# Kernel optimization log

Hardware: AMD Instinct MI355X
Metric: run time of the kernel (lower is better)

Reference implementation:

```python
import jax, jax.numpy as jnp
import numpy as np

GENETIC_CODE = {'TTT': 'F', 'TTC': 'F', 'TTA': 'L', 'TTG': 'L', 'CTT': 'L', 'CTC': 'L', 'CTA': 'L', 'CTG': 'L', 'ATT': 'I', 'ATC': 'I', 'ATA': 'I', 'ATG': 'M', 'GTT': 'V', 'GTC': 'V', 'GTA': 'V', 'GTG': 'V', 'TCT': 'S', 'TCC': 'S', 'TCA': 'S', 'TCG': 'S', 'AGT': 'S', 'AGC': 'S', 'CCT': 'P', 'CCC': 'P', 'CCA': 'P', 'CCG': 'P', 'ACT': 'T', 'ACC': 'T', 'ACA': 'T', 'ACG': 'T', 'GCT': 'A', 'GCC': 'A', 'GCA': 'A', 'GCG': 'A', 'TAT': 'Y', 'TAC': 'Y', 'TAA': '*', 'TAG': '*', 'TGA': '*', 'CAT': 'H', 'CAC': 'H', 'CAA': 'Q', 'CAG': 'Q', 'AAT': 'N', 'AAC': 'N', 'AAA': 'K', 'AAG': 'K', 'GAT': 'D', 'GAC': 'D', 'GAA': 'E', 'GAG': 'E', 'TGT': 'C', 'TGC': 'C', 'TGG': 'W', 'CGT': 'R', 'CGC': 'R', 'CGA': 'R', 'CGG': 'R', 'AGA': 'R', 'AGG': 'R', 'GGT': 'G', 'GGC': 'G', 'GGA': 'G', 'GGG': 'G'}
NUC_TO_IDX = {'T': 0, 'C': 1, 'A': 2, 'G': 3}

def _build_syn_bias(synonymy_bias=1.0):
    idx = lambda c: NUC_TO_IDX[c[0]] * 16 + NUC_TO_IDX[c[1]] * 4 + NUC_TO_IDX[c[2]]
    groups = {}
    for codon, aa in GENETIC_CODE.items():
        groups.setdefault(aa, []).append(idx(codon))
    m = np.zeros((64, 64), dtype=np.float32)
    for codons in groups.values():
        for i in codons:
            for j in codons:
                m[i, j] = synonymy_bias
    return jnp.asarray(m)

HIDDEN, N_HEADS = 256, 4
HEAD_DIM = HIDDEN // N_HEADS
B, S = 2, 4096

def setup_inputs() -> dict:
    key = jax.random.key(0)
    ks = jax.random.split(key, 10)
    std = 1.0 / np.sqrt(HIDDEN)
    lin = lambda k: jax.random.uniform(k, (HIDDEN, HIDDEN), jnp.float32, -std, std)
    bias = lambda k: jax.random.uniform(k, (HIDDEN,), jnp.float32, -std, std)
    return {
        'x': jax.random.normal(ks[0], (B, S, HIDDEN), jnp.float32),
        'codons': jax.random.randint(ks[1], (B, S), 0, 64),
        'syn_bias': _build_syn_bias(1.0),
        'wq': lin(ks[2]), 'bq': bias(ks[3]),
        'wk': lin(ks[4]), 'bk': bias(ks[5]),
        'wv': lin(ks[6]), 'bv': bias(ks[7]),
        'wo': lin(ks[8]), 'bo': bias(ks[9]),
    }

def reference(x, codons, syn_bias, wq, bq, wk, bk, wv, bv, wo, bo):
    b, s, _ = x.shape
    split = lambda t: t.reshape(b, s, N_HEADS, HEAD_DIM).transpose(0, 2, 1, 3)  # (B,H,S,D)
    q = split(x @ wq.T + bq)
    k = split(x @ wk.T + bk)
    v = split(x @ wv.T + bv)
    scores = jnp.einsum('bhqd,bhkd->bhqk', q, k) / np.sqrt(HEAD_DIM)
    # gather pairwise synonymy bias: (B,S,S) broadcast over heads
    pair_bias = syn_bias[codons[:, :, None], codons[:, None, :]]
    scores = scores + pair_bias[:, None, :, :]
    attn = jax.nn.softmax(scores, axis=-1)
    out = jnp.einsum('bhqk,bhkd->bhqd', attn, v)
    out = out.transpose(0, 2, 1, 3).reshape(b, s, HIDDEN)
    return out @ wo.T + bo
```

## Files before the change

kernel.cpp:

```cpp
#include <hip/hip_runtime.h>
#include <hip/hip_bf16.h>

#define NH 4
#define HD 64
#define HID 256
#define SS 4096
#define KP 96

#define QFRAG_PER_HEAD (128 * 6 * 64 * 8)
#define KFRAG_PER_HEAD (64 * 12 * 64 * 8)
#define VFRAG_PER_HEAD (64 * 8 * 64 * 8)

typedef float f4 __attribute__((ext_vector_type(4)));
typedef float f16v __attribute__((ext_vector_type(16)));
typedef short bf8 __attribute__((ext_vector_type(8)));
typedef unsigned int u4v __attribute__((ext_vector_type(4)));

static __device__ __forceinline__ float fast_exp2(float x) {
#if __has_builtin(__builtin_amdgcn_exp2f)
    return __builtin_amdgcn_exp2f(x);
#else
    float r; asm("v_exp_f32 %0, %1" : "=v"(r) : "v"(x)); return r;
#endif
}

static __device__ __forceinline__ unsigned pack2(float a, float b) {
    unsigned ua = (unsigned)__bfloat16_as_ushort(__float2bfloat16(a));
    unsigned ub = (unsigned)__bfloat16_as_ushort(__float2bfloat16(b));
    return ua | (ub << 16);
}

__global__ void setup_kernel(const float* __restrict__ syn,
                             int* __restrict__ gid, float* __restrict__ betaP)
{
    const int lane = threadIdx.x;
    int rep = 64;
    for (int j = 63; j >= 0; --j)
        if (syn[lane * 64 + j] != 0.0f) rep = j;
    if (rep == 64) rep = lane;
    unsigned long long m = __ballot(rep == lane);
    int id = (int)__popcll(m & ((2ull << rep) - 1ull)) - 1;
    if (id < 0) id = 0;
    gid[lane] = id;
    if (lane == 0) *betaP = syn[0] * 1.44269504088896f;
}

__global__ __launch_bounds__(256)
void pack_w_kernel(const float* __restrict__ wq, const float* __restrict__ wk,
                   const float* __restrict__ wv, const float* __restrict__ wo,
                   __hip_bfloat16* __restrict__ wpk)
{
    const int t = blockIdx.x * 256 + threadIdx.x;
    const int mat = t >> 13;
    const int r = t & 8191;
    const int dt = r >> 10, ks = (r >> 6) & 15, lane = r & 63;
    const float* w = (mat == 0) ? wq : (mat == 1) ? wk : (mat == 2) ? wv : wo;
    const int row = dt * 32 + (lane & 31);
    const int col = ks * 16 + (lane >> 5) * 8;
    const f4 a = *(const f4*)&w[(size_t)row * 256 + col];
    const f4 b = *(const f4*)&w[(size_t)row * 256 + col + 4];
    union { unsigned u[4]; bf8 v; } o;
    o.u[0] = pack2(a[0], a[1]); o.u[1] = pack2(a[2], a[3]);
    o.u[2] = pack2(b[0], b[1]); o.u[3] = pack2(b[2], b[3]);
    *(bf8*)&wpk[(size_t)t * 8] = o.v;
}

__global__ __launch_bounds__(256)
void qkv_mfma_kernel(const float* __restrict__ x,
                     const __hip_bfloat16* __restrict__ wpk,
                     const float* __restrict__ bq, const float* __restrict__ bk,
                     const float* __restrict__ bv,
                     const int* __restrict__ codons,
                     const int* __restrict__ gid, const float* __restrict__ betaP,
                     __hip_bfloat16* __restrict__ qfrag,
                     __hip_bfloat16* __restrict__ kfrag,
                     __hip_bfloat16* __restrict__ vfrag)
{
    const int bid = blockIdx.x;
    const int stile = bid / 6;
    const int grp = bid % 6;
    const int tid = threadIdx.x;
    const int w = tid >> 6, lane = tid & 63, hi = lane >> 5, l5 = lane & 31;

    const int bidx = stile >> 7;
    const int stl = stile & 127;
    const int hs = stl & 1, tkv = stl >> 1;

    __shared__ __hip_bfloat16 xs[32][256];

    {
        const int r0 = tid >> 5, c = tid & 31;
        #pragma unroll
        for (int it = 0; it < 4; ++it) {
            const int row = r0 + it * 8;
            const f4 a = *(const f4*)&x[(size_t)(stile * 32 + row) * HID + c * 8];
            const f4 b2 = *(const f4*)&x[(size_t)(stile * 32 + row) * HID + c * 8 + 4];
            union { unsigned u[4]; bf8 v; } o;
            o.u[0] = pack2(a[0], a[1]); o.u[1] = pack2(a[2], a[3]);
            o.u[2] = pack2(b2[0], b2[1]); o.u[3] = pack2(b2[2], b2[3]);
            *(bf8*)&xs[row][((c ^ row) & 31) * 8] = o.v;
        }
    }
    __syncthreads();

    const int t24 = grp * 4 + w;
    const int mat = t24 >> 3;
    const int dt = t24 & 7;
    const int head = dt >> 1, d32 = dt & 1;

    const __hip_bfloat16* wb = wpk + (size_t)((mat * 8 + dt) * 16) * 512 + (size_t)lane * 8;
    bf8 wf[16];
    #pragma unroll
    for (int ks = 0; ks < 16; ++ks) wf[ks] = *(const bf8*)&wb[ks * 512];

    f16v acc;
    #pragma unroll
    for (int r = 0; r < 16; ++r) acc[r] = 0.0f;

    if (mat < 2) {
        #pragma unroll
        for (int ks = 0; ks < 16; ++ks) {
            const bf8 xf = *(const bf8*)&xs[l5][(((ks * 2 + hi) ^ l5) & 31) * 8];
            acc = __builtin_amdgcn_mfma_f32_32x32x16_bf16(wf[ks], xf, acc, 0, 0, 0);
        }
    } else {
        #pragma unroll
        for (int ks = 0; ks < 16; ++ks) {
            const bf8 xf = *(const bf8*)&xs[l5][(((ks * 2 + hi) ^ l5) & 31) * 8];
            acc = __builtin_amdgcn_mfma_f32_32x32x16_bf16(xf, wf[ks], acc, 0, 0, 0);
        }
    }

    const float QSCALE = 0.18033688011112042f;
    if (mat == 0) {
        f4 b4[4];
        #pragma unroll
        for (int j = 0; j < 4; ++j)
            b4[j] = *(const f4*)&bq[head * 64 + d32 * 32 + j * 8 + 4 * hi];
        #pragma unroll
        for (int r = 0; r < 16; ++r) acc[r] = (acc[r] + b4[r >> 2][r & 3]) * QSCALE;
    } else if (mat == 1) {
        f4 b4[4];
        #pragma unroll
        for (int j = 0; j < 4; ++j)
            b4[j] = *(const f4*)&bk[head * 64 + d32 * 32 + j * 8 + 4 * hi];
        #pragma unroll
        for (int r = 0; r < 16; ++r) acc[r] += b4[r >> 2][r & 3];
    } else {
        const float bn = bv[head * 64 + d32 * 32 + l5];
        #pragma unroll
        for (int r = 0; r < 16; ++r) acc[r] += bn;
    }

    unsigned wd[8];
    #pragma unroll
    for (int i = 0; i < 8; ++i) wd[i] = pack2(acc[2 * i], acc[2 * i + 1]);
    const unsigned e0 = (unsigned)__shfl_xor((int)(hi ? wd[0] : wd[2]), 32, 64);
    const unsigned e1 = (unsigned)__shfl_xor((int)(hi ? wd[1] : wd[3]), 32, 64);
    const unsigned e2 = (unsigned)__shfl_xor((int)(hi ? wd[4] : wd[6]), 32, 64);
    const unsigned e3 = (unsigned)__shfl_xor((int)(hi ? wd[5] : wd[7]), 32, 64);
    union { unsigned u[4]; bf8 v; } fa, fb;
    if (hi == 0) {
        fa.u[0] = wd[0]; fa.u[1] = wd[1]; fa.u[2] = e0; fa.u[3] = e1;
        fb.u[0] = wd[4]; fb.u[1] = wd[5]; fb.u[2] = e2; fb.u[3] = e3;
    } else {
        fa.u[0] = e0; fa.u[1] = e1; fa.u[2] = wd[2]; fa.u[3] = wd[3];
        fb.u[0] = e2; fb.u[1] = e3; fb.u[2] = wd[6]; fb.u[3] = wd[7];
    }

    const int hd = bidx * NH + head;
    if (mat == 0) {
        __hip_bfloat16* qb = qfrag + (size_t)hd * QFRAG_PER_HEAD;
        *(bf8*)&qb[((size_t)(stl * 6 + d32 * 2 + 0) * 64 + lane) * 8] = fa.v;
        *(bf8*)&qb[((size_t)(stl * 6 + d32 * 2 + 1) * 64 + lane) * 8] = fb.v;
    } else if (mat == 1) {
        __hip_bfloat16* kb = kfrag + (size_t)hd * KFRAG_PER_HEAD;
        *(bf8*)&kb[((size_t)(tkv * 12 + d32 * 4 + hs) * 64 + lane) * 8] = fa.v;
        *(bf8*)&kb[((size_t)(tkv * 12 + d32 * 4 + 2 + hs) * 64 + lane) * 8] = fb.v;
    } else {
        __hip_bfloat16* vb = vfrag + (size_t)hd * VFRAG_PER_HEAD;
        const int ja = ((stl * 2 + 0) & 3) * 2 + d32;
        const int jb = ((stl * 2 + 1) & 3) * 2 + d32;
        *(bf8*)&vb[((size_t)(tkv * 8 + ja) * 64 + lane) * 8] = fa.v;
        *(bf8*)&vb[((size_t)(tkv * 8 + jb) * 64 + lane) * 8] = fb.v;
    }

    if (grp == 0) {
        const int hh = w;
        const int hd2 = bidx * NH + hh;
        __hip_bfloat16* qb = qfrag + (size_t)hd2 * QFRAG_PER_HEAD;
        __hip_bfloat16* kb = kfrag + (size_t)hd2 * KFRAG_PER_HEAD;
        u4v z; z[0] = 0; z[1] = 0; z[2] = 0; z[3] = 0;
        *(u4v*)&qb[((size_t)(stl * 6 + 4) * 64 + lane) * 8] = z;
        *(u4v*)&qb[((size_t)(stl * 6 + 5) * 64 + lane) * 8] = z;
        *(u4v*)&kb[((size_t)(tkv * 12 + 8 + hs) * 64 + lane) * 8] = z;
        *(u4v*)&kb[((size_t)(tkv * 12 + 10 + hs) * 64 + lane) * 8] = z;
        asm volatile("s_waitcnt vmcnt(0)" ::: "memory");
        if (hi == 0) {
            const int cg = gid[codons[bidx * SS + stl * 32 + l5] & 63];
            const float bl2e = *betaP;
            const int lt = ((cg >> 3) & 1) * 32 + l5;
            qb[((size_t)(stl * 6 + 4 + (cg >> 4)) * 64 + lt) * 8 + (cg & 7)] =
                __float2bfloat16(bl2e);
            kb[((size_t)(tkv * 12 + 8 + (cg >> 4) * 2 + hs) * 64 + lt) * 8 + (cg & 7)] =
                __float2bfloat16(1.0f);
        }
    }
}

__global__ __launch_bounds__(256, 2)
void attn_kernel(const __hip_bfloat16* __restrict__ qfrag,
                 const __hip_bfloat16* __restrict__ kfrag,
                 const __hip_bfloat16* __restrict__ vfrag,
                 __hip_bfloat16* __restrict__ aoutb)
{
    const int bid = blockIdx.x;
    const int bh = bid & 7;
    const int b = bh >> 2, h = bh & 3;
    const int qtile = bid >> 3;
    const int tid = threadIdx.x;
    const int w = tid >> 6;
    const int lane = tid & 63;
    const int q5 = lane & 31;
    const int hi = lane >> 5;

    __shared__ float o_sh[4][32][69];
    __shared__ float l_sh[4][32];

    const __hip_bfloat16* kf_base = kfrag + (size_t)(b * NH + h) * KFRAG_PER_HEAD + lane * 8;
    const __hip_bfloat16* vf_base = vfrag + (size_t)(b * NH + h) * VFRAG_PER_HEAD + lane * 8;

    const __hip_bfloat16* qb = qfrag + (size_t)(b * NH + h) * QFRAG_PER_HEAD
                               + ((size_t)qtile * 6 * 64 + lane) * 8;
    bf8 qf[6];
    #pragma unroll
    for (int ks = 0; ks < 6; ++ks)
        qf[ks] = *(const bf8*)&qb[ks * 512];

    f16v oacc0, oacc1;
    #pragma unroll
    for (int r = 0; r < 16; ++r) { oacc0[r] = 0.0f; oacc1[r] = 0.0f; }
    float lrun = 0.0f;

    bf8 kA[12], kB[12];

    auto loadK = [&](bf8 (&dst)[12], int tt) {
        const __hip_bfloat16* p = kf_base + (size_t)tt * (12 * 64 * 8);
        #pragma unroll
        for (int j = 0; j < 12; ++j) dst[j] = *(const bf8*)&p[j * 512];
    };

    auto step = [&](bf8 (&kf)[12], bf8 (&kn)[12], int tt, bool pf) {
        bf8 vf[8];
        const __hip_bfloat16* vp = vf_base + (size_t)tt * (8 * 64 * 8);
        #pragma unroll
        for (int j = 0; j < 8; ++j) vf[j] = *(const bf8*)&vp[j * 512];
        if (pf) loadK(kn, tt + 1);

        f16v sA, sB;
        #pragma unroll
        for (int r = 0; r < 16; ++r) { sA[r] = 0.0f; sB[r] = 0.0f; }
        __builtin_amdgcn_s_setprio(1);
        #pragma unroll
        for (int ks = 0; ks < 6; ++ks) {
            sA = __builtin_amdgcn_mfma_f32_32x32x16_bf16(kf[ks * 2 + 0], qf[ks], sA, 0, 0, 0);
            sB = __builtin_amdgcn_mfma_f32_32x32x16_bf16(kf[ks * 2 + 1], qf[ks], sB, 0, 0, 0);
        }
        __builtin_amdgcn_s_setprio(0);

        float ls = 0.0f;
        #pragma unroll
        for (int r = 0; r < 16; ++r) { sA[r] = fast_exp2(sA[r]); ls += sA[r]; }
        #pragma unroll
        for (int r = 0; r < 16; ++r) { sB[r] = fast_exp2(sB[r]); ls += sB[r]; }
        lrun += ls;

        unsigned dwv[2][4][2];
        #pragma unroll
        for (int j = 0; j < 4; ++j)
            #pragma unroll
            for (int c = 0; c < 2; ++c) {
                dwv[0][j][c] = pack2(sA[j * 4 + 2 * c], sA[j * 4 + 2 * c + 1]);
                dwv[1][j][c] = pack2(sB[j * 4 + 2 * c], sB[j * 4 + 2 * c + 1]);
            }
        unsigned rc[2][2][2];
        #pragma unroll
        for (int t2 = 0; t2 < 2; ++t2)
            #pragma unroll
            for (int k1 = 0; k1 < 2; ++k1)
                #pragma unroll
                for (int c = 0; c < 2; ++c) {
                    const unsigned snd = hi ? dwv[t2][2 * k1][c] : dwv[t2][2 * k1 + 1][c];
                    rc[t2][k1][c] = (unsigned)__shfl_xor((int)snd, 32, 64);
                }

        __builtin_amdgcn_s_setprio(1);
        #pragma unroll
        for (int ks = 0; ks < 4; ++ks) {
            const int t2 = ks >> 1, k1 = ks & 1;
            union { unsigned u[4]; bf8 v; } pfv;
            pfv.u[0] = hi ? rc[t2][k1][0] : dwv[t2][2 * k1][0];
            pfv.u[1] = hi ? rc[t2][k1][1] : dwv[t2][2 * k1][1];
            pfv.u[2] = hi ? dwv[t2][2 * k1 + 1][0] : rc[t2][k1][0];
            pfv.u[3] = hi ? dwv[t2][2 * k1 + 1][1] : rc[t2][k1][1];
            oacc0 = __builtin_amdgcn_mfma_f32_32x32x16_bf16(vf[ks * 2 + 0], pfv.v, oacc0, 0, 0, 0);
            oacc1 = __builtin_amdgcn_mfma_f32_32x32x16_bf16(vf[ks * 2 + 1], pfv.v, oacc1, 0, 0, 0);
        }
        __builtin_amdgcn_s_setprio(0);
    };

    const int tt0 = w * 16;
    loadK(kA, tt0);
    #pragma unroll 1
    for (int t = 0; t < 16; t += 2) {
        step(kA, kB, tt0 + t, true);
        step(kB, kA, tt0 + t + 1, t + 2 < 16);
    }

    const float ltot = lrun + __shfl_xor(lrun, 32, 64);
    #pragma unroll
    for (int r = 0; r < 16; ++r) {
        const int d = (r & 3) + 8 * (r >> 2) + 4 * hi;
        o_sh[w][q5][d] = oacc0[r];
        o_sh[w][q5][32 + d] = oacc1[r];
    }
    if (hi == 0) l_sh[w][q5] = ltot;
    __syncthreads();

    const int row = tid >> 3;
    const int d0 = (tid & 7) * 8;
    const float inv = 1.0f / (l_sh[0][row] + l_sh[1][row] + l_sh[2][row] + l_sh[3][row]);
    float vals[8];
    #pragma unroll
    for (int j = 0; j < 8; ++j)
        vals[j] = (o_sh[0][row][d0 + j] + o_sh[1][row][d0 + j]
                 + o_sh[2][row][d0 + j] + o_sh[3][row][d0 + j]) * inv;
    union { unsigned u[4]; bf8 v; } ov;
    ov.u[0] = pack2(vals[0], vals[1]); ov.u[1] = pack2(vals[2], vals[3]);
    ov.u[2] = pack2(vals[4], vals[5]); ov.u[3] = pack2(vals[6], vals[7]);
    *(bf8*)&aoutb[((size_t)b * SS + qtile * 32 + row) * HID + h * HD + d0] = ov.v;
}

__global__ __launch_bounds__(256)
void out_proj_kernel(const __hip_bfloat16* __restrict__ aoutb,
                     const __hip_bfloat16* __restrict__ wpk,
                     const float* __restrict__ bo, float* __restrict__ out)
{
    const int bid = blockIdx.x;
    const int stile = bid >> 1, grp = bid & 1;
    const int tid = threadIdx.x;
    const int w = tid >> 6, lane = tid & 63, hi = lane >> 5, l5 = lane & 31;

    __shared__ __hip_bfloat16 xs[32][256];
    {
        const int r0 = tid >> 5, c = tid & 31;
        #pragma unroll
        for (int it = 0; it < 4; ++it) {
            const int row = r0 + it * 8;
            const bf8 v = *(const bf8*)&aoutb[(size_t)(stile * 32 + row) * HID + c * 8];
            *(bf8*)&xs[row][((c ^ row) & 31) * 8] = v;
        }
    }
    __syncthreads();

    const int nt = grp * 4 + w;
    const __hip_bfloat16* wb = wpk + (size_t)((3 * 8 + nt) * 16) * 512 + (size_t)lane * 8;
    bf8 wf[16];
    #pragma unroll
    for (int ks = 0; ks < 16; ++ks) wf[ks] = *(const bf8*)&wb[ks * 512];

    f16v acc;
    #pragma unroll
    for (int r = 0; r < 16; ++r) acc[r] = 0.0f;
    #pragma unroll
    for (int ks = 0; ks < 16; ++ks) {
        const bf8 xf = *(const bf8*)&xs[l5][(((ks * 2 + hi) ^ l5) & 31) * 8];
        acc = __builtin_amdgcn_mfma_f32_32x32x16_bf16(xf, wf[ks], acc, 0, 0, 0);
    }

    const float bn = bo[nt * 32 + l5];
    #pragma unroll
    for (int r = 0; r < 16; ++r) {
        const int sloc = (r & 3) + 8 * (r >> 2) + 4 * hi;
        out[(size_t)(stile * 32 + sloc) * HID + nt * 32 + l5] = acc[r] + bn;
    }
}

extern "C" void kernel_launch(void* const* d_in, const int* in_sizes, int n_in,
                              void* d_out, int out_size, void* d_ws, size_t ws_size,
                              hipStream_t stream)
{
    (void)in_sizes; (void)n_in; (void)out_size; (void)ws_size;
    const float* x        = (const float*)d_in[0];
    const int*   codons   = (const int*)d_in[1];
    const float* syn_bias = (const float*)d_in[2];
    const float* wq = (const float*)d_in[3];
    const float* bq = (const float*)d_in[4];
    const float* wk = (const float*)d_in[5];
    const float* bk = (const float*)d_in[6];
    const float* wv = (const float*)d_in[7];
    const float* bv = (const float*)d_in[8];
    const float* wo = (const float*)d_in[9];
    const float* bo = (const float*)d_in[10];
    float* out = (float*)d_out;

    char* ws = (char*)d_ws;
    int*   gid   = (int*)(ws);
    float* betaP = (float*)(ws + 256);
    __hip_bfloat16* wpk   = (__hip_bfloat16*)(ws + 4096);
    __hip_bfloat16* qfrag = (__hip_bfloat16*)(ws + (size_t)1048576u);
    __hip_bfloat16* kfrag = (__hip_bfloat16*)(ws + (size_t)7340032u);
    __hip_bfloat16* vfrag = (__hip_bfloat16*)(ws + (size_t)13631488u);
    __hip_bfloat16* aoutb = (__hip_bfloat16*)(ws + (size_t)17825792u);

    setup_kernel<<<1, 64, 0, stream>>>(syn_bias, gid, betaP);
    pack_w_kernel<<<128, 256, 0, stream>>>(wq, wk, wv, wo, wpk);
    qkv_mfma_kernel<<<1536, 256, 0, stream>>>(x, wpk, bq, bk, bv, codons, gid, betaP,
                                              qfrag, kfrag, vfrag);
    attn_kernel<<<1024, 256, 0, stream>>>(qfrag, kfrag, vfrag, aoutb);
    out_proj_kernel<<<512, 256, 0, stream>>>(aoutb, wpk, bo, out);
}
```

Measured before the change: 90.93 us.

## Process two query tiles per attention block to reuse K/V fragments

Each attention block now handles 64 queries (two 32-row tiles) instead of 32. Every loaded K and V fragment feeds both tiles, which halves global K/V traffic per query, and the grid shrinks from 1024 to 512 blocks. The K double buffer is replaced by a single buffer that is refilled after the second score MFMA. The trade-off is more accumulator registers, a larger shared-memory reduction buffer, and fewer blocks, which may lower occupancy and latency hiding.

```diff
diff --git a/kernel.cpp b/kernel.cpp
--- a/kernel.cpp
+++ b/kernel.cpp
@@ -217,64 +217,45 @@
     const int bid = blockIdx.x;
     const int bh = bid & 7;
     const int b = bh >> 2, h = bh & 3;
-    const int qtile = bid >> 3;
+    const int qg = bid >> 3;
     const int tid = threadIdx.x;
     const int w = tid >> 6;
     const int lane = tid & 63;
     const int q5 = lane & 31;
     const int hi = lane >> 5;
 
-    __shared__ float o_sh[4][32][69];
-    __shared__ float l_sh[4][32];
+    __shared__ float o_sh[4][64][69];
+    __shared__ float l_sh[4][64];
 
     const __hip_bfloat16* kf_base = kfrag + (size_t)(b * NH + h) * KFRAG_PER_HEAD + lane * 8;
     const __hip_bfloat16* vf_base = vfrag + (size_t)(b * NH + h) * VFRAG_PER_HEAD + lane * 8;
 
     const __hip_bfloat16* qb = qfrag + (size_t)(b * NH + h) * QFRAG_PER_HEAD
-                               + ((size_t)qtile * 6 * 64 + lane) * 8;
-    bf8 qf[6];
-    #pragma unroll
-    for (int ks = 0; ks < 6; ++ks)
-        qf[ks] = *(const bf8*)&qb[ks * 512];
-
-    f16v oacc0, oacc1;
-    #pragma unroll
-    for (int r = 0; r < 16; ++r) { oacc0[r] = 0.0f; oacc1[r] = 0.0f; }
-    float lrun = 0.0f;
-
-    bf8 kA[12], kB[12];
-
-    auto loadK = [&](bf8 (&dst)[12], int tt) {
+                               + ((size_t)(qg * 2) * 6 * 64 + lane) * 8;
+    bf8 qf0[6], qf1[6];
+    #pragma unroll
+    for (int ks = 0; ks < 6; ++ks) {
+        qf0[ks] = *(const bf8*)&qb[ks * 512];
+        qf1[ks] = *(const bf8*)&qb[3072 + ks * 512];
+    }
+
+    f16v oacc00, oacc01, oacc10, oacc11;
+    #pragma unroll
+    for (int r = 0; r < 16; ++r) {
+        oacc00[r] = 0.0f; oacc01[r] = 0.0f; oacc10[r] = 0.0f; oacc11[r] = 0.0f;
+    }
+    float lrun0 = 0.0f, lrun1 = 0.0f;
+
+    bf8 kf[12];
+    const int tt0 = w * 16;
+
+    auto loadK = [&](int tt) {
         const __hip_bfloat16* p = kf_base + (size_t)tt * (12 * 64 * 8);
         #pragma unroll
-        for (int j = 0; j < 12; ++j) dst[j] = *(const bf8*)&p[j * 512];
+        for (int j = 0; j < 12; ++j) kf[j] = *(const bf8*)&p[j * 512];
     };
 
-    auto step = [&](bf8 (&kf)[12], bf8 (&kn)[12], int tt, bool pf) {
-        bf8 vf[8];
-        const __hip_bfloat16* vp = vf_base + (size_t)tt * (8 * 64 * 8);
-        #pragma unroll
-        for (int j = 0; j < 8; ++j) vf[j] = *(const bf8*)&vp[j * 512];
-        if (pf) loadK(kn, tt + 1);
-
-        f16v sA, sB;
-        #pragma unroll
-        for (int r = 0; r < 16; ++r) { sA[r] = 0.0f; sB[r] = 0.0f; }
-        __builtin_amdgcn_s_setprio(1);
-        #pragma unroll
-        for (int ks = 0; ks < 6; ++ks) {
-            sA = __builtin_amdgcn_mfma_f32_32x32x16_bf16(kf[ks * 2 + 0], qf[ks], sA, 0, 0, 0);
-            sB = __builtin_amdgcn_mfma_f32_32x32x16_bf16(kf[ks * 2 + 1], qf[ks], sB, 0, 0, 0);
-        }
-        __builtin_amdgcn_s_setprio(0);
-
-        float ls = 0.0f;
-        #pragma unroll
-        for (int r = 0; r < 16; ++r) { sA[r] = fast_exp2(sA[r]); ls += sA[r]; }
-        #pragma unroll
-        for (int r = 0; r < 16; ++r) { sB[r] = fast_exp2(sB[r]); ls += sB[r]; }
-        lrun += ls;
-
+    auto packP = [&](const f16v& sA, const f16v& sB, bf8 (&pfv)[4]) {
         unsigned dwv[2][4][2];
         #pragma unroll
         for (int j = 0; j < 4; ++j)
@@ -293,52 +274,110 @@
                     const unsigned snd = hi ? dwv[t2][2 * k1][c] : dwv[t2][2 * k1 + 1][c];
                     rc[t2][k1][c] = (unsigned)__shfl_xor((int)snd, 32, 64);
                 }
-
-        __builtin_amdgcn_s_setprio(1);
         #pragma unroll
         for (int ks = 0; ks < 4; ++ks) {
             const int t2 = ks >> 1, k1 = ks & 1;
-            union { unsigned u[4]; bf8 v; } pfv;
-            pfv.u[0] = hi ? rc[t2][k1][0] : dwv[t2][2 * k1][0];
-            pfv.u[1] = hi ? rc[t2][k1][1] : dwv[t2][2 * k1][1];
-            pfv.u[2] = hi ? dwv[t2][2 * k1 + 1][0] : rc[t2][k1][0];
-            pfv.u[3] = hi ? dwv[t2][2 * k1 + 1][1] : rc[t2][k1][1];
-            oacc0 = __builtin_amdgcn_mfma_f32_32x32x16_bf16(vf[ks * 2 + 0], pfv.v, oacc0, 0, 0, 0);
-            oacc1 = __builtin_amdgcn_mfma_f32_32x32x16_bf16(vf[ks * 2 + 1], pfv.v, oacc1, 0, 0, 0);
+            union { unsigned u[4]; bf8 v; } pu;
+            pu.u[0] = hi ? rc[t2][k1][0] : dwv[t2][2 * k1][0];
+            pu.u[1] = hi ? rc[t2][k1][1] : dwv[t2][2 * k1][1];
+            pu.u[2] = hi ? dwv[t2][2 * k1 + 1][0] : rc[t2][k1][0];
+            pu.u[3] = hi ? dwv[t2][2 * k1 + 1][1] : rc[t2][k1][1];
+            pfv[ks] = pu.v;
+        }
+    };
+
+    loadK(tt0);
+
+    #pragma unroll 1
+    for (int t = 0; t < 16; ++t) {
+        const int tt = tt0 + t;
+
+        bf8 vf[8];
+        const __hip_bfloat16* vp = vf_base + (size_t)tt * (8 * 64 * 8);
+        #pragma unroll
+        for (int j = 0; j < 8; ++j) vf[j] = *(const bf8*)&vp[j * 512];
+
+        f16v sA, sB;
+        #pragma unroll
+        for (int r = 0; r < 16; ++r) { sA[r] = 0.0f; sB[r] = 0.0f; }
+        __builtin_amdgcn_s_setprio(1);
+        #pragma unroll
+        for (int ks = 0; ks < 6; ++ks) {
+            sA = __builtin_amdgcn_mfma_f32_32x32x16_bf16(kf[ks * 2 + 0], qf0[ks], sA, 0, 0, 0);
+            sB = __builtin_amdgcn_mfma_f32_32x32x16_bf16(kf[ks * 2 + 1], qf0[ks], sB, 0, 0, 0);
         }
         __builtin_amdgcn_s_setprio(0);
-    };
-
-    const int tt0 = w * 16;
-    loadK(kA, tt0);
-    #pragma unroll 1
-    for (int t = 0; t < 16; t += 2) {
-        step(kA, kB, tt0 + t, true);
-        step(kB, kA, tt0 + t + 1, t + 2 < 16);
-    }
-
-    const float ltot = lrun + __shfl_xor(lrun, 32, 64);
+
+        float ls0 = 0.0f;
+        #pragma unroll
+        for (int r = 0; r < 16; ++r) { sA[r] = fast_exp2(sA[r]); ls0 += sA[r]; }
+        #pragma unroll
+        for (int r = 0; r < 16; ++r) { sB[r] = fast_exp2(sB[r]); ls0 += sB[r]; }
+        lrun0 += ls0;
+        bf8 pfv0[4];
+        packP(sA, sB, pfv0);
+
+        #pragma unroll
+        for (int r = 0; r < 16; ++r) { sA[r] = 0.0f; sB[r] = 0.0f; }
+        __builtin_amdgcn_s_setprio(1);
+        #pragma unroll
+        for (int ks = 0; ks < 6; ++ks) {
+            sA = __builtin_amdgcn_mfma_f32_32x32x16_bf16(kf[ks * 2 + 0], qf1[ks], sA, 0, 0, 0);
+            sB = __builtin_amdgcn_mfma_f32_32x32x16_bf16(kf[ks * 2 + 1], qf1[ks], sB, 0, 0, 0);
+        }
+        __builtin_amdgcn_s_setprio(0);
+
+        if (t + 1 < 16) loadK(tt + 1);
+
+        float ls1 = 0.0f;
+        #pragma unroll
+        for (int r = 0; r < 16; ++r) { sA[r] = fast_exp2(sA[r]); ls1 += sA[r]; }
+        #pragma unroll
+        for (int r = 0; r < 16; ++r) { sB[r] = fast_exp2(sB[r]); ls1 += sB[r]; }
+        lrun1 += ls1;
+        bf8 pfv1[4];
+        packP(sA, sB, pfv1);
+
+        __builtin_amdgcn_s_setprio(1);
+        #pragma unroll
+        for (int ks = 0; ks < 4; ++ks) {
+            oacc00 = __builtin_amdgcn_mfma_f32_32x32x16_bf16(vf[ks * 2 + 0], pfv0[ks], oacc00, 0, 0, 0);
+            oacc01 = __builtin_amdgcn_mfma_f32_32x32x16_bf16(vf[ks * 2 + 1], pfv0[ks], oacc01, 0, 0, 0);
+            oacc10 = __builtin_amdgcn_mfma_f32_32x32x16_bf16(vf[ks * 2 + 0], pfv1[ks], oacc10, 0, 0, 0);
+            oacc11 = __builtin_amdgcn_mfma_f32_32x32x16_bf16(vf[ks * 2 + 1], pfv1[ks], oacc11, 0, 0, 0);
+        }
+        __builtin_amdgcn_s_setprio(0);
+    }
+
+    const float ltot0 = lrun0 + __shfl_xor(lrun0, 32, 64);
+    const float ltot1 = lrun1 + __shfl_xor(lrun1, 32, 64);
     #pragma unroll
     for (int r = 0; r < 16; ++r) {
         const int d = (r & 3) + 8 * (r >> 2) + 4 * hi;
-        o_sh[w][q5][d] = oacc0[r];
-        o_sh[w][q5][32 + d] = oacc1[r];
-    }
-    if (hi == 0) l_sh[w][q5] = ltot;
+        o_sh[w][q5][d] = oacc00[r];
+        o_sh[w][q5][32 + d] = oacc01[r];
+        o_sh[w][32 + q5][d] = oacc10[r];
+        o_sh[w][32 + q5][32 + d] = oacc11[r];
+    }
+    if (hi == 0) { l_sh[w][q5] = ltot0; l_sh[w][32 + q5] = ltot1; }
     __syncthreads();
 
-    const int row = tid >> 3;
-    const int d0 = (tid & 7) * 8;
+    const int row = tid >> 2;
+    const int d0 = (tid & 3) * 16;
     const float inv = 1.0f / (l_sh[0][row] + l_sh[1][row] + l_sh[2][row] + l_sh[3][row]);
-    float vals[8];
-    #pragma unroll
-    for (int j = 0; j < 8; ++j)
+    float vals[16];
+    #pragma unroll
+    for (int j = 0; j < 16; ++j)
         vals[j] = (o_sh[0][row][d0 + j] + o_sh[1][row][d0 + j]
                  + o_sh[2][row][d0 + j] + o_sh[3][row][d0 + j]) * inv;
-    union { unsigned u[4]; bf8 v; } ov;
-    ov.u[0] = pack2(vals[0], vals[1]); ov.u[1] = pack2(vals[2], vals[3]);
-    ov.u[2] = pack2(vals[4], vals[5]); ov.u[3] = pack2(vals[6], vals[7]);
-    *(bf8*)&aoutb[((size_t)b * SS + qtile * 32 + row) * HID + h * HD + d0] = ov.v;
+    union { unsigned u[4]; bf8 v; } ov0, ov1;
+    ov0.u[0] = pack2(vals[0], vals[1]);   ov0.u[1] = pack2(vals[2], vals[3]);
+    ov0.u[2] = pack2(vals[4], vals[5]);   ov0.u[3] = pack2(vals[6], vals[7]);
+    ov1.u[0] = pack2(vals[8], vals[9]);   ov1.u[1] = pack2(vals[10], vals[11]);
+    ov1.u[2] = pack2(vals[12], vals[13]); ov1.u[3] = pack2(vals[14], vals[15]);
+    __hip_bfloat16* dst = &aoutb[((size_t)b * SS + qg * 64 + row) * HID + h * HD + d0];
+    *(bf8*)&dst[0] = ov0.v;
+    *(bf8*)&dst[8] = ov1.v;
 }
 
 __global__ __launch_bounds__(256)
@@ -417,6 +456,6 @@
     pack_w_kernel<<<128, 256, 0, stream>>>(wq, wk, wv, wo, wpk);
     qkv_mfma_kernel<<<1536, 256, 0, stream>>>(x, wpk, bq, bk, bv, codons, gid, betaP,
                                               qfrag, kfrag, vfrag);
-    attn_kernel<<<1024, 256, 0, stream>>>(qfrag, kfrag, vfrag, aoutb);
+    attn_kernel<<<512, 256, 0, stream>>>(qfrag, kfrag, vfrag, aoutb);
     out_proj_kernel<<<512, 256, 0, stream>>>(aoutb, wpk, bo, out);
 }
```

Measured after the change: 102.8 us. 1.13x slower.

## Share K/V tiles across waves via LDS and split KV range into two halves

Applied to the files above, without the earlier changes.

The attention kernel now has each wave own a separate 32-query tile. The four waves cooperatively stage each K/V tile into double-buffered shared memory, replacing per-wave global reloads of the same K/V fragments. The key range is split across two blocks that write unnormalized bf16 partial outputs and row sums. The output projection sums these partials and normalizes them. This cuts redundant global K/V traffic by sharing it across waves, at the cost of per-tile __syncthreads, extra LDS reads, and a second partial buffer with extra bf16 rounding of the unnormalized sums.

```diff
diff --git a/kernel.cpp b/kernel.cpp
--- a/kernel.cpp
+++ b/kernel.cpp
@@ -5,7 +5,6 @@
 #define HD 64
 #define HID 256
 #define SS 4096
-#define KP 96
 
 #define QFRAG_PER_HEAD (128 * 6 * 64 * 8)
 #define KFRAG_PER_HEAD (64 * 12 * 64 * 8)
@@ -212,50 +211,73 @@
 void attn_kernel(const __hip_bfloat16* __restrict__ qfrag,
                  const __hip_bfloat16* __restrict__ kfrag,
                  const __hip_bfloat16* __restrict__ vfrag,
-                 __hip_bfloat16* __restrict__ aoutb)
+                 __hip_bfloat16* __restrict__ po0,
+                 __hip_bfloat16* __restrict__ po1,
+                 float* __restrict__ ls0,
+                 float* __restrict__ ls1)
 {
     const int bid = blockIdx.x;
     const int bh = bid & 7;
     const int b = bh >> 2, h = bh & 3;
-    const int qtile = bid >> 3;
+    const int idx = bid >> 3;
+    const int half = idx & 1;
+    const int qg = idx >> 1;
     const int tid = threadIdx.x;
     const int w = tid >> 6;
     const int lane = tid & 63;
     const int q5 = lane & 31;
     const int hi = lane >> 5;
 
-    __shared__ float o_sh[4][32][69];
-    __shared__ float l_sh[4][32];
-
-    const __hip_bfloat16* kf_base = kfrag + (size_t)(b * NH + h) * KFRAG_PER_HEAD + lane * 8;
-    const __hip_bfloat16* vf_base = vfrag + (size_t)(b * NH + h) * VFRAG_PER_HEAD + lane * 8;
-
+    __shared__ __align__(16) char smem[40960];
+    __shared__ float l_sh[128];
+
+    const char* kT = (const char*)(kfrag + (size_t)(b * NH + h) * KFRAG_PER_HEAD);
+    const char* vT = (const char*)(vfrag + (size_t)(b * NH + h) * VFRAG_PER_HEAD);
+
+    const int stl = qg * 4 + w;
     const __hip_bfloat16* qb = qfrag + (size_t)(b * NH + h) * QFRAG_PER_HEAD
-                               + ((size_t)qtile * 6 * 64 + lane) * 8;
+                               + ((size_t)stl * 6 * 64 + lane) * 8;
     bf8 qf[6];
     #pragma unroll
-    for (int ks = 0; ks < 6; ++ks)
-        qf[ks] = *(const bf8*)&qb[ks * 512];
+    for (int ks = 0; ks < 6; ++ks) qf[ks] = *(const bf8*)&qb[ks * 512];
 
     f16v oacc0, oacc1;
     #pragma unroll
     for (int r = 0; r < 16; ++r) { oacc0[r] = 0.0f; oacc1[r] = 0.0f; }
     float lrun = 0.0f;
 
-    bf8 kA[12], kB[12];
-
-    auto loadK = [&](bf8 (&dst)[12], int tt) {
-        const __hip_bfloat16* p = kf_base + (size_t)tt * (12 * 64 * 8);
-        #pragma unroll
-        for (int j = 0; j < 12; ++j) dst[j] = *(const bf8*)&p[j * 512];
+    const int w5 = w * 5;
+    bf8 g[5];
+
+    auto loadG = [&](int tt) {
+        #pragma unroll
+        for (int c = 0; c < 5; ++c) {
+            const int id = w5 + c;
+            const char* src = (id < 12)
+                ? kT + (size_t)tt * 12288 + (size_t)id * 1024
+                : vT + (size_t)tt * 8192 + (size_t)(id - 12) * 1024;
+            g[c] = *(const bf8*)(src + lane * 16);
+        }
     };
-
-    auto step = [&](bf8 (&kf)[12], bf8 (&kn)[12], int tt, bool pf) {
-        bf8 vf[8];
-        const __hip_bfloat16* vp = vf_base + (size_t)tt * (8 * 64 * 8);
-        #pragma unroll
-        for (int j = 0; j < 8; ++j) vf[j] = *(const bf8*)&vp[j * 512];
-        if (pf) loadK(kn, tt + 1);
+    auto writeL = [&](int buf) {
+        #pragma unroll
+        for (int c = 0; c < 5; ++c) {
+            const int id = w5 + c;
+            *(bf8*)&smem[buf * 20480 + id * 1024 + lane * 16] = g[c];
+        }
+    };
+
+    const int tt0 = half * 32;
+    loadG(tt0);
+    writeL(0);
+    __syncthreads();
+
+    int cur = 0;
+    #pragma unroll 1
+    for (int t = 0; t < 32; ++t) {
+        if (t + 1 < 32) loadG(tt0 + t + 1);
+
+        const char* kb = smem + cur * 20480 + lane * 16;
 
         f16v sA, sB;
         #pragma unroll
@@ -263,8 +285,10 @@
         __builtin_amdgcn_s_setprio(1);
         #pragma unroll
         for (int ks = 0; ks < 6; ++ks) {
-            sA = __builtin_amdgcn_mfma_f32_32x32x16_bf16(kf[ks * 2 + 0], qf[ks], sA, 0, 0, 0);
-            sB = __builtin_amdgcn_mfma_f32_32x32x16_bf16(kf[ks * 2 + 1], qf[ks], sB, 0, 0, 0);
+            const bf8 k0 = *(const bf8*)(kb + (2 * ks) * 1024);
+            const bf8 k1 = *(const bf8*)(kb + (2 * ks + 1) * 1024);
+            sA = __builtin_amdgcn_mfma_f32_32x32x16_bf16(k0, qf[ks], sA, 0, 0, 0);
+            sB = __builtin_amdgcn_mfma_f32_32x32x16_bf16(k1, qf[ks], sB, 0, 0, 0);
         }
         __builtin_amdgcn_s_setprio(0);
 
@@ -293,56 +317,67 @@
                     const unsigned snd = hi ? dwv[t2][2 * k1][c] : dwv[t2][2 * k1 + 1][c];
                     rc[t2][k1][c] = (unsigned)__shfl_xor((int)snd, 32, 64);
                 }
-
-        __builtin_amdgcn_s_setprio(1);
+        bf8 pfv[4];
         #pragma unroll
         for (int ks = 0; ks < 4; ++ks) {
             const int t2 = ks >> 1, k1 = ks & 1;
-            union { unsigned u[4]; bf8 v; } pfv;
-            pfv.u[0] = hi ? rc[t2][k1][0] : dwv[t2][2 * k1][0];
-            pfv.u[1] = hi ? rc[t2][k1][1] : dwv[t2][2 * k1][1];
-            pfv.u[2] = hi ? dwv[t2][2 * k1 + 1][0] : rc[t2][k1][0];
-            pfv.u[3] = hi ? dwv[t2][2 * k1 + 1][1] : rc[t2][k1][1];
-            oacc0 = __builtin_amdgcn_mfma_f32_32x32x16_bf16(vf[ks * 2 + 0], pfv.v, oacc0, 0, 0, 0);
-            oacc1 = __builtin_amdgcn_mfma_f32_32x32x16_bf16(vf[ks * 2 + 1], pfv.v, oacc1, 0, 0, 0);
+            union { unsigned u[4]; bf8 v; } pu;
+            pu.u[0] = hi ? rc[t2][k1][0] : dwv[t2][2 * k1][0];
+            pu.u[1] = hi ? rc[t2][k1][1] : dwv[t2][2 * k1][1];
+            pu.u[2] = hi ? dwv[t2][2 * k1 + 1][0] : rc[t2][k1][0];
+            pu.u[3] = hi ? dwv[t2][2 * k1 + 1][1] : rc[t2][k1][1];
+            pfv[ks] = pu.v;
+        }
+
+        __builtin_amdgcn_s_setprio(1);
+        #pragma unroll
+        for (int ks = 0; ks < 4; ++ks) {
+            const bf8 v0 = *(const bf8*)(kb + (12 + 2 * ks) * 1024);
+            const bf8 v1 = *(const bf8*)(kb + (13 + 2 * ks) * 1024);
+            oacc0 = __builtin_amdgcn_mfma_f32_32x32x16_bf16(v0, pfv[ks], oacc0, 0, 0, 0);
+            oacc1 = __builtin_amdgcn_mfma_f32_32x32x16_bf16(v1, pfv[ks], oacc1, 0, 0, 0);
         }
         __builtin_amdgcn_s_setprio(0);
-    };
-
-    const int tt0 = w * 16;
-    loadK(kA, tt0);
-    #pragma unroll 1
-    for (int t = 0; t < 16; t += 2) {
-        step(kA, kB, tt0 + t, true);
-        step(kB, kA, tt0 + t + 1, t + 2 < 16);
+
+        if (t + 1 < 32) writeL(cur ^ 1);
+        __syncthreads();
+        cur ^= 1;
     }
 
     const float ltot = lrun + __shfl_xor(lrun, 32, 64);
+    float* osh = (float*)smem;
     #pragma unroll
     for (int r = 0; r < 16; ++r) {
         const int d = (r & 3) + 8 * (r >> 2) + 4 * hi;
-        o_sh[w][q5][d] = oacc0[r];
-        o_sh[w][q5][32 + d] = oacc1[r];
-    }
-    if (hi == 0) l_sh[w][q5] = ltot;
+        osh[(w * 32 + q5) * 68 + d] = oacc0[r];
+        osh[(w * 32 + q5) * 68 + 32 + d] = oacc1[r];
+    }
+    if (hi == 0) l_sh[w * 32 + q5] = ltot;
     __syncthreads();
 
-    const int row = tid >> 3;
-    const int d0 = (tid & 7) * 8;
-    const float inv = 1.0f / (l_sh[0][row] + l_sh[1][row] + l_sh[2][row] + l_sh[3][row]);
-    float vals[8];
-    #pragma unroll
-    for (int j = 0; j < 8; ++j)
-        vals[j] = (o_sh[0][row][d0 + j] + o_sh[1][row][d0 + j]
-                 + o_sh[2][row][d0 + j] + o_sh[3][row][d0 + j]) * inv;
-    union { unsigned u[4]; bf8 v; } ov;
-    ov.u[0] = pack2(vals[0], vals[1]); ov.u[1] = pack2(vals[2], vals[3]);
-    ov.u[2] = pack2(vals[4], vals[5]); ov.u[3] = pack2(vals[6], vals[7]);
-    *(bf8*)&aoutb[((size_t)b * SS + qtile * 32 + row) * HID + h * HD + d0] = ov.v;
+    __hip_bfloat16* pob = half ? po1 : po0;
+    float* lsb = half ? ls1 : ls0;
+    const int row = tid >> 1;
+    const int dh = (tid & 1) * 32;
+    const float* src = &osh[row * 68 + dh];
+    __hip_bfloat16* dst = pob + ((size_t)(b * SS + qg * 128 + row) * HID + h * HD + dh);
+    #pragma unroll
+    for (int j = 0; j < 4; ++j) {
+        const f4 x0 = *(const f4*)&src[j * 8];
+        const f4 x1 = *(const f4*)&src[j * 8 + 4];
+        union { unsigned u[4]; bf8 v; } o;
+        o.u[0] = pack2(x0[0], x0[1]); o.u[1] = pack2(x0[2], x0[3]);
+        o.u[2] = pack2(x1[0], x1[1]); o.u[3] = pack2(x1[2], x1[3]);
+        *(bf8*)&dst[j * 8] = o.v;
+    }
+    if (tid < 128) lsb[(size_t)(b * SS + qg * 128 + tid) * 4 + h] = l_sh[tid];
 }
 
 __global__ __launch_bounds__(256)
-void out_proj_kernel(const __hip_bfloat16* __restrict__ aoutb,
+void out_proj_kernel(const __hip_bfloat16* __restrict__ po0,
+                     const __hip_bfloat16* __restrict__ po1,
+                     const float* __restrict__ ls0,
+                     const float* __restrict__ ls1,
                      const __hip_bfloat16* __restrict__ wpk,
                      const float* __restrict__ bo, float* __restrict__ out)
 {
@@ -357,8 +392,22 @@
         #pragma unroll
         for (int it = 0; it < 4; ++it) {
             const int row = r0 + it * 8;
-            const bf8 v = *(const bf8*)&aoutb[(size_t)(stile * 32 + row) * HID + c * 8];
-            *(bf8*)&xs[row][((c ^ row) & 31) * 8] = v;
+            const size_t srow = (size_t)stile * 32 + row;
+            const int head = c >> 3;
+            const float inv = 1.0f / (ls0[srow * 4 + head] + ls1[srow * 4 + head]);
+            union { bf8 v; unsigned u[4]; } a0, a1;
+            a0.v = *(const bf8*)&po0[srow * 256 + c * 8];
+            a1.v = *(const bf8*)&po1[srow * 256 + c * 8];
+            union { unsigned u[4]; bf8 v; } o;
+            #pragma unroll
+            for (int i = 0; i < 4; ++i) {
+                const float lo = __uint_as_float(a0.u[i] << 16)
+                               + __uint_as_float(a1.u[i] << 16);
+                const float hv = __uint_as_float(a0.u[i] & 0xffff0000u)
+                               + __uint_as_float(a1.u[i] & 0xffff0000u);
+                o.u[i] = pack2(lo * inv, hv * inv);
+            }
+            *(bf8*)&xs[row][((c ^ row) & 31) * 8] = o.v;
         }
     }
     __syncthreads();
@@ -411,12 +460,15 @@
     __hip_bfloat16* qfrag = (__hip_bfloat16*)(ws + (size_t)1048576u);
     __hip_bfloat16* kfrag = (__hip_bfloat16*)(ws + (size_t)7340032u);
     __hip_bfloat16* vfrag = (__hip_bfloat16*)(ws + (size_t)13631488u);
-    __hip_bfloat16* aoutb = (__hip_bfloat16*)(ws + (size_t)17825792u);
+    __hip_bfloat16* po0   = (__hip_bfloat16*)(ws + (size_t)17825792u);
+    __hip_bfloat16* po1   = (__hip_bfloat16*)(ws + (size_t)22020096u);
+    float* ls0            = (float*)(ws + (size_t)26214400u);
+    float* ls1            = (float*)(ws + (size_t)26345472u);
 
     setup_kernel<<<1, 64, 0, stream>>>(syn_bias, gid, betaP);
     pack_w_kernel<<<128, 256, 0, stream>>>(wq, wk, wv, wo, wpk);
     qkv_mfma_kernel<<<1536, 256, 0, stream>>>(x, wpk, bq, bk, bv, codons, gid, betaP,
                                               qfrag, kfrag, vfrag);
-    attn_kernel<<<1024, 256, 0, stream>>>(qfrag, kfrag, vfrag, aoutb);
-    out_proj_kernel<<<512, 256, 0, stream>>>(aoutb, wpk, bo, out);
-}
+    attn_kernel<<<512, 256, 0, stream>>>(qfrag, kfrag, vfrag, po0, po1, ls0, ls1);
+    out_proj_kernel<<<512, 256, 0, stream>>>(po0, po1, ls0, ls1, wpk, bo, out);
+}
```

New measurement: 84.17 us. 7.4% less time.
